# Kernel tuning notes

Hardware: AMD Instinct MI355X
Metric: run time of the kernel (lower is better)

The kernel has to match this reference:

```python
import jax, jax.numpy as jnp
from jax import lax
import numpy as np

D_MODEL = 512
H = 4
DK = 128
DV = 256
DFF = 2048
N_LAYERS = 12
N_LOC = 100  # 10x10 patches

CONV_SPECS = [(8, 3, 3), (16, 8, 3), (32, 16, 3), (32, 32, 3), (64, 32, 3),
              (64, 64, 3), (128, 64, 3), (128, 128, 3), (256, 128, 3), (512, 256, 2)]
RELU_AFTER = [False, True, False, True, True, True, True, True, True, False]


def setup_inputs() -> dict:
    key = jax.random.key(0)
    keys = iter(jax.random.split(key, 64))

    def nrm(shape, scale=0.02):
        return jax.random.normal(next(keys), shape, dtype=jnp.float32) * scale

    inp = {"x": jax.random.normal(next(keys), (1, 3, 200, 200), dtype=jnp.float32)}
    for i, (o, c, k) in enumerate(CONV_SPECS, 1):
        inp[f"cw{i}"] = nrm((o, c, k, k))
        inp[f"cb{i}"] = nrm((o,))
    inp["Wq"] = nrm((N_LAYERS, H, D_MODEL, DK))
    inp["Wk"] = nrm((N_LAYERS, H, D_MODEL, DK))
    inp["Wv"] = nrm((N_LAYERS, H, D_MODEL, DV))
    inp["Wo"] = nrm((N_LAYERS, H * DV, D_MODEL))
    inp["W1"] = nrm((N_LAYERS, D_MODEL, DFF))
    inp["b1"] = nrm((N_LAYERS, DFF))
    inp["W2"] = nrm((N_LAYERS, DFF, D_MODEL))
    inp["b2"] = nrm((N_LAYERS, D_MODEL))
    return inp


def _extract_patches(x):
    # x: [1,3,200,200] -> 100 patches of [3,20,20], index = i*10 + j
    # patch(i,j) = x[:, :, 20j:20(j+1), 20i:20(i+1)]  (i=cols outer, j=rows inner)
    x = x.reshape(3, 10, 20, 10, 20)            # [c, j_blk, row, i_blk, col]
    return jnp.transpose(x, (3, 1, 0, 2, 4)).reshape(N_LOC, 3, 20, 20)


def _local_embed(patches, cws, cbs):
    h = patches  # [100,3,20,20]
    for w, b, r in zip(cws, cbs, RELU_AFTER):
        h = lax.conv_general_dilated(h, w, (1, 1), 'VALID',
                                     dimension_numbers=('NCHW', 'OIHW', 'NCHW'))
        h = h + b[None, :, None, None]
        if r:
            h = jax.nn.relu(h)
    return h.reshape(N_LOC, D_MODEL)  # spatial reduced to 1x1


def _location_embeddings():
    # createLocationEmbedding(i, j) only uses i (the column-block coordinate).
    pos = jnp.repeat(jnp.arange(0, 200, 20, dtype=jnp.float32), 10)  # [100]
    k = jnp.arange(256, dtype=jnp.float32)
    inv = jnp.power(jnp.float32(10000.0), 2.0 * k / 256.0)
    ang = pos[:, None] / inv[None, :]  # [100,256]
    return jnp.concatenate([jnp.sin(ang), jnp.cos(ang)], axis=1)  # [100,512]


def _encoder_layer(h, Wq, Wk, Wv, Wo, W1, b1, W2, b2):
    # Multi-head attention; NOTE: scale uses K.size(0) = n_locations (faithful quirk).
    scale = 1.0 / jnp.sqrt(jnp.float32(N_LOC))
    q = jnp.einsum('nd,hdk->hnk', h, Wq)
    k = jnp.einsum('nd,hdk->hnk', h, Wk)
    v = jnp.einsum('nd,hdv->hnv', h, Wv)
    s = jnp.einsum('hnk,hmk->hnm', q, k) * scale
    a = jax.nn.softmax(s, axis=-1)
    o = jnp.einsum('hnm,hmv->hnv', a, v)
    o = jnp.transpose(o, (1, 0, 2)).reshape(N_LOC, H * DV)
    h = h + o @ Wo
    h = h + (jax.nn.relu(h @ W1 + b1) @ W2 + b2)
    return h


def reference(x, cw1, cb1, cw2, cb2, cw3, cb3, cw4, cb4, cw5, cb5,
              cw6, cb6, cw7, cb7, cw8, cb8, cw9, cb9, cw10, cb10,
              Wq, Wk, Wv, Wo, W1, b1, W2, b2):
    cws = [cw1, cw2, cw3, cw4, cw5, cw6, cw7, cw8, cw9, cw10]
    cbs = [cb1, cb2, cb3, cb4, cb5, cb6, cb7, cb8, cb9, cb10]
    patches = _extract_patches(x)
    h = _local_embed(patches, cws, cbs)
    h = h + _location_embeddings()
    for n in range(N_LAYERS):
        h = _encoder_layer(h, Wq[n], Wk[n], Wv[n], Wo[n], W1[n], b1[n], W2[n], b2[n])
    return h
```

## Files before the change

### kernel.cpp

```cpp
#include <hip/hip_runtime.h>
#include <math.h>

#define NLOC 100

typedef __attribute__((ext_vector_type(8))) _Float16 half8;
typedef __attribute__((ext_vector_type(4))) float f32x4;

#define XP_OFF    0
#define H_OFF     160000
#define QKV_OFF   211200
#define OCAT_OFF  416000
#define FFN_OFF   467200
#define ACTA_OFF  569600
#define ACTB_OFF  889664
#define CWH_OFF   1209728
#define CW1_OFF   1765504
#define WQKVT_OFF 1765824
#define WOT_OFF   8057280
#define W1T_OFF   11203008
#define W2T_OFF   17494464

struct WPack { const float* w[9]; };

__global__ __launch_bounds__(256) void stage_xp(const float* __restrict__ x, float* __restrict__ xp)
{
    int idx = blockIdx.x*256 + threadIdx.x;
    if (idx >= 160000) return;
    int c = idx & 3;
    int idx2 = idx >> 2;
    int p = idx2 / 400;
    int rr = idx2 - p*400;
    int y = rr / 20, xx = rr - y*20;
    int pi = p/10, pj = p - pi*10;
    float v = 0.f;
    if (c < 3) v = x[c*40000 + (pj*20 + y)*200 + pi*20 + xx];
    xp[idx] = v;
}

__global__ __launch_bounds__(256) void cw1repack(const float* __restrict__ w, float* __restrict__ w4)
{
    int idx = threadIdx.x;
    if (idx >= 288) return;
    int c = idx & 3;
    int r = idx >> 2;
    int oc = r / 9, kk = r - oc*9;
    int ky = kk/3, kx = kk - ky*3;
    float v = 0.f;
    if (c < 3) v = w[((oc*3 + c)*3 + ky)*3 + kx];
    w4[idx] = v;
}

__global__ __launch_bounds__(256) void cwrepack(WPack wp, unsigned short* __restrict__ dst)
{
    const int Cin[9]  = {8,16,32,32,64,64,128,128,256};
    const int shift[9]= {3,4,5,5,6,6,7,7,8};
    const int KS[9]   = {3,3,3,3,3,3,3,3,2};
    const int Kpad[9] = {96,160,288,288,576,576,1152,1152,1024};
    const int off[10] = {0,1536,6656,15872,34304,71168,144896,292352,587264,1111552};
    const int total = 1111552;
    for (int i = blockIdx.x*blockDim.x + threadIdx.x; i < total; i += gridDim.x*blockDim.x) {
        int l = 0;
        while (i >= off[l+1]) ++l;
        int rem = i - off[l];
        int kp = Kpad[l];
        int oc = rem / kp;
        int k  = rem - oc*kp;
        int ci = Cin[l];
        int ic = k & (ci - 1);
        int kk = k >> shift[l];
        int ks = KS[l], k2 = ks*ks;
        float v = 0.f;
        if (kk < k2) {
            int ky = kk / ks, kx = kk - ky*ks;
            v = wp.w[l][((oc*ci + ic)*ks + ky)*ks + kx];
        }
        _Float16 hv = (_Float16)v;
        dst[i] = __builtin_bit_cast(unsigned short, hv);
    }
}

__global__ __launch_bounds__(256) void conv1k(const float4* __restrict__ xp4,
    const float4* __restrict__ w4, const float* __restrict__ bias, unsigned short* __restrict__ out)
{
    int idx = blockIdx.x*256 + threadIdx.x;
    if (idx >= 259200) return;
    int oc = idx & 7;
    int r = idx >> 3;
    int p = r / 324;
    int s = r - p*324;
    int sy = s / 18, sx = s - sy*18;
    const float4* ip = xp4 + (size_t)(p*20 + sy)*20 + sx;
    float acc = 0.f;
    #pragma unroll
    for (int ky = 0; ky < 3; ++ky)
        #pragma unroll
        for (int kx = 0; kx < 3; ++kx) {
            float4 iv = ip[ky*20 + kx];
            float4 wv = w4[oc*9 + ky*3 + kx];
            acc += iv.x*wv.x + iv.y*wv.y + iv.z*wv.z;
        }
    acc += bias[oc];
    _Float16 hv = (_Float16)acc;
    out[idx] = __builtin_bit_cast(unsigned short, hv);
}

template<int CIN, int COUT, int KS, int HIN, int WIN, int HOUT, int WOUT, int KPAD, int RELU, int LAST>
__global__ __launch_bounds__(256) void convM(const unsigned short* __restrict__ in,
    const unsigned short* __restrict__ wth, const float* __restrict__ bias,
    unsigned short* __restrict__ out, float* __restrict__ hout)
{
    constexpr int HW = HOUT*WOUT;
    constexpr int M = 100*HW;
    constexpr int MT = (M + 15)/16;
    constexpr int NT = COUT/16;
    int wave = threadIdx.x >> 6, lane = threadIdx.x & 63;
    int t = blockIdx.x*4 + wave;
    if (t >= MT*NT) return;
    int mt = t % MT, nt = t / MT;
    int mrow = lane & 15, quad = lane >> 4;
    int mg = mt*16 + mrow; if (mg >= M) mg = M - 1;
    int p = mg / HW, s = mg - p*HW;
    int sy = s / WOUT, sx = s - sy*WOUT;
    const unsigned short* ap = in + ((size_t)((p*HIN + sy)*WIN + sx))*CIN;
    const unsigned short* bp = wth + ((size_t)(nt*16 + mrow))*KPAD + quad*8;
    f32x4 acc = {0.f, 0.f, 0.f, 0.f};
    #pragma unroll
    for (int k0 = 0; k0 < KPAD; k0 += 32) {
        int k = k0 + quad*8;
        int kk = k / CIN; if (kk > KS*KS - 1) kk = KS*KS - 1;
        int ky = kk / KS, kx = kk - ky*KS;
        uint4 av = *(const uint4*)(ap + (ky*WIN + kx)*CIN + (k & (CIN-1)));
        uint4 bv = *(const uint4*)(bp + k0);
        acc = __builtin_amdgcn_mfma_f32_16x16x32_f16(
            __builtin_bit_cast(half8, av), __builtin_bit_cast(half8, bv), acc, 0, 0, 0);
    }
    int n = nt*16 + mrow;
    float bv = bias[n];
    #pragma unroll
    for (int r = 0; r < 4; ++r) {
        int m = mt*16 + quad*4 + r;
        if (m < M) {
            float v = acc[r] + bv;
            if (RELU) v = fmaxf(v, 0.f);
            if (LAST) {
                int pi = m / 10;
                float pos = 20.f * (float)pi;
                int dd = n & 255;
                float inv = powf(10000.f, (float)dd * (1.f/128.f));
                float ang = pos / inv;
                v += (n < 256) ? sinf(ang) : cosf(ang);
                hout[(size_t)m*512 + n] = v;
            } else {
                _Float16 hv = (_Float16)v;
                out[(size_t)m*COUT + n] = __builtin_bit_cast(unsigned short, hv);
            }
        }
    }
}

__global__ __launch_bounds__(256) void wtrans(
    const float* __restrict__ src, unsigned short* __restrict__ dst,
    int K, int N, int matsPerLayer, int dstLayerStride, int dstBase)
{
    __shared__ float t[32][33];
    int mz = blockIdx.z;
    int layer = mz / matsPerLayer;
    int mi = mz - layer*matsPerLayer;
    const float* s = src + (size_t)mz * K * N;
    unsigned short* d = dst + (size_t)layer*dstLayerStride + dstBase + (size_t)mi * N * K;
    int n0 = blockIdx.x*32, k0 = blockIdx.y*32;
    int tx = threadIdx.x & 31, ty = threadIdx.x >> 5;
    #pragma unroll
    for (int i = 0; i < 32; i += 8) t[ty + i][tx] = s[(size_t)(k0 + ty + i)*N + n0 + tx];
    __syncthreads();
    #pragma unroll
    for (int i = 0; i < 32; i += 8) {
        _Float16 hv = (_Float16)t[tx][ty + i];
        d[(size_t)(n0 + ty + i)*K + k0 + tx] = __builtin_bit_cast(unsigned short, hv);
    }
}

template<int ABITS, int RELU, int ATOMIC, int STOREH>
__global__ __launch_bounds__(256) void gemm16(
    const void* __restrict__ Av, int lda,
    const unsigned short* __restrict__ Bt, int K,
    const float* __restrict__ bias,
    float* __restrict__ C, unsigned short* __restrict__ Ch, int ldc,
    int kchunk)
{
    int lane = threadIdx.x & 63;
    int wave = threadIdx.x >> 6;
    int mrow = lane & 15, quad = lane >> 4;
    int n0 = blockIdx.x*64 + wave*16;
    int m0 = blockIdx.y*16;
    int arow = m0 + mrow; if (arow > 99) arow = 99;
    int k0 = blockIdx.z * kchunk;
    const unsigned short* bp = Bt + (size_t)(n0 + mrow)*K + quad*8 + k0;
    f32x4 acc = {0.f, 0.f, 0.f, 0.f};
    if (ABITS == 16) {
        const unsigned short* ap = (const unsigned short*)Av + (size_t)arow*lda + quad*8 + k0;
        for (int k = 0; k < kchunk; k += 32) {
            uint4 au = *(const uint4*)(ap + k);
            uint4 bu = *(const uint4*)(bp + k);
            acc = __builtin_amdgcn_mfma_f32_16x16x32_f16(
                __builtin_bit_cast(half8, au), __builtin_bit_cast(half8, bu), acc, 0, 0, 0);
        }
    } else {
        const float* ap = (const float*)Av + (size_t)arow*lda + quad*8 + k0;
        for (int k = 0; k < kchunk; k += 32) {
            float4 f0 = *(const float4*)(ap + k);
            float4 f1 = *(const float4*)(ap + k + 4);
            half8 af;
            af[0] = (_Float16)f0.x; af[1] = (_Float16)f0.y;
            af[2] = (_Float16)f0.z; af[3] = (_Float16)f0.w;
            af[4] = (_Float16)f1.x; af[5] = (_Float16)f1.y;
            af[6] = (_Float16)f1.z; af[7] = (_Float16)f1.w;
            uint4 bu = *(const uint4*)(bp + k);
            acc = __builtin_amdgcn_mfma_f32_16x16x32_f16(
                af, __builtin_bit_cast(half8, bu), acc, 0, 0, 0);
        }
    }
    int n = n0 + mrow;
    float bv = (bias != nullptr && blockIdx.z == 0) ? bias[n] : 0.f;
    #pragma unroll
    for (int r = 0; r < 4; ++r) {
        int row = m0 + quad*4 + r;
        if (row < 100) {
            float v = acc[r] + bv;
            if (RELU) v = fmaxf(v, 0.f);
            if (ATOMIC) atomicAdd(&C[(size_t)row*ldc + n], v);
            else if (C != nullptr) C[(size_t)row*ldc + n] = v;
            if (STOREH) {
                _Float16 hv = (_Float16)v;
                Ch[(size_t)row*ldc + n] = __builtin_bit_cast(unsigned short, hv);
            }
        }
    }
}

__global__ __launch_bounds__(256) void attn_kernel(
    const float* __restrict__ qkv, unsigned short* __restrict__ ocat)
{
    __shared__ float qr[128];
    __shared__ float p[100];
    __shared__ float red[2];
    int bx = blockIdx.x;
    int hh = bx / 100, nn = bx - hh*100;
    int t = threadIdx.x;
    if (t < 128) qr[t] = qkv[(size_t)nn*2048 + hh*128 + t];
    __syncthreads();
    float sv = 0.f;
    if (t < 100) {
        const float4* kp = (const float4*)(qkv + (size_t)t*2048 + 512 + hh*128);
        const float4* q4 = (const float4*)qr;
        float s0=0.f, s1=0.f, s2=0.f, s3=0.f;
        #pragma unroll 8
        for (int j = 0; j < 32; ++j) {
            float4 a = q4[j], b = kp[j];
            s0 += a.x*b.x; s1 += a.y*b.y; s2 += a.z*b.z; s3 += a.w*b.w;
        }
        sv = (s0+s1+s2+s3) * 0.1f;
        p[t] = sv;
    }
    __syncthreads();
    if (t < 64) {
        float m = fmaxf(p[t], (t+64 < 100) ? p[t+64] : -1e30f);
        for (int o = 32; o > 0; o >>= 1) m = fmaxf(m, __shfl_down(m, o));
        if (t == 0) red[0] = m;
    }
    __syncthreads();
    float mx = red[0];
    if (t < 100) p[t] = expf(sv - mx);
    __syncthreads();
    if (t < 64) {
        float s = p[t] + ((t+64 < 100) ? p[t+64] : 0.f);
        for (int o = 32; o > 0; o >>= 1) s += __shfl_down(s, o);
        if (t == 0) red[1] = s;
    }
    __syncthreads();
    float inv = 1.0f / red[1];
    const float* vp = qkv + 1024 + hh*256 + t;
    float acc = 0.f;
    #pragma unroll 4
    for (int m = 0; m < 100; ++m) acc += p[m] * vp[(size_t)m*2048];
    _Float16 hv = (_Float16)(acc * inv);
    ocat[(size_t)nn*1024 + hh*256 + t] = __builtin_bit_cast(unsigned short, hv);
}

__global__ __launch_bounds__(256) void copyk(const float* __restrict__ s, float* __restrict__ d, int n)
{
    int i = blockIdx.x*256 + threadIdx.x;
    if (i < n) d[i] = s[i];
}

extern "C" void kernel_launch(void* const* d_in, const int* in_sizes, int n_in,
                              void* d_out, int out_size, void* d_ws, size_t ws_size,
                              hipStream_t stream)
{
    const float* x = (const float*)d_in[0];
    const float* cw1 = (const float*)d_in[1];
    const float* cb[10];
    WPack wpk;
    for (int i = 0; i < 10; ++i) cb[i] = (const float*)d_in[2 + 2*i];
    for (int i = 0; i < 9; ++i)  wpk.w[i] = (const float*)d_in[3 + 2*i];
    const float* Wq = (const float*)d_in[21];
    const float* Wk = (const float*)d_in[22];
    const float* Wv = (const float*)d_in[23];
    const float* Wo = (const float*)d_in[24];
    const float* W1 = (const float*)d_in[25];
    const float* b1 = (const float*)d_in[26];
    const float* W2 = (const float*)d_in[27];
    const float* b2 = (const float*)d_in[28];

    float* ws = (float*)d_ws;
    float* xp  = ws + XP_OFF;
    float* h   = ws + H_OFF;
    float* qkv = ws + QKV_OFF;
    unsigned short* ocat = (unsigned short*)(ws + OCAT_OFF);
    unsigned short* ffn  = (unsigned short*)(ws + FFN_OFF);
    unsigned short* aA   = (unsigned short*)(ws + ACTA_OFF);
    unsigned short* aB   = (unsigned short*)(ws + ACTB_OFF);
    unsigned short* cwh  = (unsigned short*)(ws + CWH_OFF);
    float* cw14 = ws + CW1_OFF;
    unsigned short* wqkvt = (unsigned short*)(ws + WQKVT_OFF);
    unsigned short* wot   = (unsigned short*)(ws + WOT_OFF);
    unsigned short* w1t   = (unsigned short*)(ws + W1T_OFF);
    unsigned short* w2t   = (unsigned short*)(ws + W2T_OFF);

    cw1repack<<<2, 256, 0, stream>>>(cw1, cw14);
    cwrepack<<<2172, 256, 0, stream>>>(wpk, cwh);
    wtrans<<<dim3(4, 16, 48),  256, 0, stream>>>(Wq, wqkvt, 512, 128,  4, 2048*512, 0);
    wtrans<<<dim3(4, 16, 48),  256, 0, stream>>>(Wk, wqkvt, 512, 128,  4, 2048*512, 512*512);
    wtrans<<<dim3(8, 16, 48),  256, 0, stream>>>(Wv, wqkvt, 512, 256,  4, 2048*512, 1024*512);
    wtrans<<<dim3(16, 32, 12), 256, 0, stream>>>(Wo, wot,  1024, 512,  1, 512*1024, 0);
    wtrans<<<dim3(64, 16, 12), 256, 0, stream>>>(W1, w1t,   512, 2048, 1, 2048*512, 0);
    wtrans<<<dim3(16, 64, 12), 256, 0, stream>>>(W2, w2t,  2048, 512,  1, 512*2048, 0);

    stage_xp<<<625, 256, 0, stream>>>(x, xp);
    conv1k<<<1013, 256, 0, stream>>>((const float4*)xp, (const float4*)cw14, cb[0], aA);
    convM<8,  16, 3,18,18,16,16,  96,1,0><<<400, 256, 0, stream>>>(aA, cwh + 0,      cb[1], aB, nullptr);
    convM<16, 32, 3,16,16,14,14, 160,0,0><<<613, 256, 0, stream>>>(aB, cwh + 1536,   cb[2], aA, nullptr);
    convM<32, 32, 3,14,14,12,12, 288,1,0><<<450, 256, 0, stream>>>(aA, cwh + 6656,   cb[3], aB, nullptr);
    convM<32, 64, 3,12,12,10,10, 288,1,0><<<625, 256, 0, stream>>>(aB, cwh + 15872,  cb[4], aA, nullptr);
    convM<64, 64, 3,10,10, 8, 8, 576,1,0><<<400, 256, 0, stream>>>(aA, cwh + 34304,  cb[5], aB, nullptr);
    convM<64,128, 3, 8, 8, 6, 6, 576,1,0><<<450, 256, 0, stream>>>(aB, cwh + 71168,  cb[6], aA, nullptr);
    convM<128,128,3, 6, 6, 4, 4,1152,1,0><<<200, 256, 0, stream>>>(aA, cwh + 144896, cb[7], aB, nullptr);
    convM<128,256,3, 4, 4, 2, 2,1152,1,0><<<100, 256, 0, stream>>>(aB, cwh + 292352, cb[8], aA, nullptr);
    convM<256,512,2, 2, 2, 1, 1,1024,0,1><<<56,  256, 0, stream>>>(aA, cwh + 587264, cb[9], nullptr, h);

    for (int n = 0; n < 12; ++n) {
        const unsigned short* Bq  = wqkvt + (size_t)n * 2048 * 512;
        const unsigned short* Bo  = wot   + (size_t)n * 512 * 1024;
        const unsigned short* Bf1 = w1t   + (size_t)n * 2048 * 512;
        const unsigned short* Bf2 = w2t   + (size_t)n * 512 * 2048;
        gemm16<32,0,0,0><<<dim3(32, 7, 1), 256, 0, stream>>>(h, 512, Bq, 512,
            nullptr, qkv, nullptr, 2048, 512);
        attn_kernel<<<400, 256, 0, stream>>>(qkv, ocat);
        gemm16<16,0,1,0><<<dim3(8, 7, 4), 256, 0, stream>>>(ocat, 1024, Bo, 1024,
            nullptr, h, nullptr, 512, 256);
        gemm16<32,1,0,1><<<dim3(32, 7, 1), 256, 0, stream>>>(h, 512, Bf1, 512,
            b1 + (size_t)n*2048, nullptr, ffn, 2048, 512);
        gemm16<16,0,1,0><<<dim3(8, 7, 8), 256, 0, stream>>>(ffn, 2048, Bf2, 2048,
            b2 + (size_t)n*512, h, nullptr, 512, 256);
    }
    copyk<<<200, 256, 0, stream>>>(h, (float*)d_out, NLOC*512);
}
```

Measured before the change: 880.8 us.

## Merge weight prep into one kernel, fuse attention with output projection

Replaces the conv weight repack and six transpose kernels with a single grid-stride prep kernel that transposes with vectorized stores. Folds patch staging into the first conv. Fuses attention with the Wo projection and residual add, using one 1024-thread block per query row. That block also writes an fp16 copy of h, so the FFN1 GEMM reads half-precision input. The aim is fewer launches and less intermediate traffic, but the fused Wo projection now runs as scalar FMAs over only 100 blocks instead of MFMA tiles.

Result: slower. 1.213 ms (+37.7%).

```diff
diff --git a/kernel.cpp b/kernel.cpp
--- a/kernel.cpp
+++ b/kernel.cpp
@@ -6,15 +6,13 @@
 typedef __attribute__((ext_vector_type(8))) _Float16 half8;
 typedef __attribute__((ext_vector_type(4))) float f32x4;
 
-#define XP_OFF    0
 #define H_OFF     160000
 #define QKV_OFF   211200
-#define OCAT_OFF  416000
+#define H16_OFF   416000
 #define FFN_OFF   467200
 #define ACTA_OFF  569600
 #define ACTB_OFF  889664
 #define CWH_OFF   1209728
-#define CW1_OFF   1765504
 #define WQKVT_OFF 1765824
 #define WOT_OFF   8057280
 #define W1T_OFF   11203008
@@ -22,66 +20,115 @@
 
 struct WPack { const float* w[9]; };
 
-__global__ __launch_bounds__(256) void stage_xp(const float* __restrict__ x, float* __restrict__ xp)
-{
-    int idx = blockIdx.x*256 + threadIdx.x;
-    if (idx >= 160000) return;
-    int c = idx & 3;
-    int idx2 = idx >> 2;
-    int p = idx2 / 400;
-    int rr = idx2 - p*400;
-    int y = rr / 20, xx = rr - y*20;
-    int pi = p/10, pj = p - pi*10;
-    float v = 0.f;
-    if (c < 3) v = x[c*40000 + (pj*20 + y)*200 + pi*20 + xx];
-    xp[idx] = v;
-}
-
-__global__ __launch_bounds__(256) void cw1repack(const float* __restrict__ w, float* __restrict__ w4)
-{
-    int idx = threadIdx.x;
-    if (idx >= 288) return;
-    int c = idx & 3;
-    int r = idx >> 2;
-    int oc = r / 9, kk = r - oc*9;
-    int ky = kk/3, kx = kk - ky*3;
-    float v = 0.f;
-    if (c < 3) v = w[((oc*3 + c)*3 + ky)*3 + kx];
-    w4[idx] = v;
-}
-
-__global__ __launch_bounds__(256) void cwrepack(WPack wp, unsigned short* __restrict__ dst)
-{
-    const int Cin[9]  = {8,16,32,32,64,64,128,128,256};
-    const int shift[9]= {3,4,5,5,6,6,7,7,8};
-    const int KS[9]   = {3,3,3,3,3,3,3,3,2};
-    const int Kpad[9] = {96,160,288,288,576,576,1152,1152,1024};
-    const int off[10] = {0,1536,6656,15872,34304,71168,144896,292352,587264,1111552};
-    const int total = 1111552;
-    for (int i = blockIdx.x*blockDim.x + threadIdx.x; i < total; i += gridDim.x*blockDim.x) {
-        int l = 0;
-        while (i >= off[l+1]) ++l;
-        int rem = i - off[l];
-        int kp = Kpad[l];
-        int oc = rem / kp;
-        int k  = rem - oc*kp;
-        int ci = Cin[l];
-        int ic = k & (ci - 1);
-        int kk = k >> shift[l];
-        int ks = KS[l], k2 = ks*ks;
+struct TJob {
+    const float* src; unsigned short* dst;
+    int K, N, mpl, lstride, base, tiles;
+};
+
+struct PrepParams {
+    WPack wpk;
+    const float* Wq; const float* Wk; const float* Wv; const float* Wo;
+    const float* W1; const float* W2;
+    float* ws;
+};
+
+__global__ __launch_bounds__(256) void prep_all(PrepParams PP)
+{
+    float* ws = PP.ws;
+    unsigned short* cwh   = (unsigned short*)(ws + CWH_OFF);
+    unsigned short* wqkvt = (unsigned short*)(ws + WQKVT_OFF);
+    unsigned short* wot   = (unsigned short*)(ws + WOT_OFF);
+    unsigned short* w1t   = (unsigned short*)(ws + W1T_OFF);
+    unsigned short* w2t   = (unsigned short*)(ws + W2T_OFF);
+
+    const int tid = threadIdx.x;
+    const int gthread = blockIdx.x*256 + tid;
+    const int nthreads = gridDim.x*256;
+    const int gwave = gthread >> 6;
+    const int nwaves = nthreads >> 6;
+    const int lane = tid & 63;
+
+    __shared__ TJob jobs[6];
+    if (tid == 0) {
+        jobs[0] = TJob{PP.Wq, wqkvt,  512,  128, 4, 2048*512, 0,        1536};
+        jobs[1] = TJob{PP.Wk, wqkvt,  512,  128, 4, 2048*512, 512*512,  1536};
+        jobs[2] = TJob{PP.Wv, wqkvt,  512,  256, 4, 2048*512, 1024*512, 3072};
+        jobs[3] = TJob{PP.Wo, wot,   1024,  512, 1, 512*1024, 0,        3072};
+        jobs[4] = TJob{PP.W1, w1t,    512, 2048, 1, 2048*512, 0,        6144};
+        jobs[5] = TJob{PP.W2, w2t,   2048,  512, 1, 512*2048, 0,        6144};
+    }
+    __syncthreads();
+
+    {
+        const int Cin[9]   = {8,16,32,32,64,64,128,128,256};
+        const int shiftv[9]= {3,4,5,5,6,6,7,7,8};
+        const int KSa[9]   = {3,3,3,3,3,3,3,3,2};
+        const int Kpad[9]  = {96,160,288,288,576,576,1152,1152,1024};
+        const int off[10]  = {0,1536,6656,15872,34304,71168,144896,292352,587264,1111552};
+        for (int i = gthread; i < 1111552; i += nthreads) {
+            int l = 0;
+            while (i >= off[l+1]) ++l;
+            int rem = i - off[l];
+            int kp = Kpad[l];
+            int oc = rem / kp;
+            int k  = rem - oc*kp;
+            int ci = Cin[l];
+            int ic = k & (ci - 1);
+            int kk = k >> shiftv[l];
+            int ks = KSa[l], k2 = ks*ks;
+            float v = 0.f;
+            if (kk < k2) {
+                int ky = kk / ks, kx = kk - ky*ks;
+                v = PP.wpk.w[l][((oc*ci + ic)*ks + ky)*ks + kx];
+            }
+            _Float16 hv = (_Float16)v;
+            cwh[i] = __builtin_bit_cast(unsigned short, hv);
+        }
+    }
+    for (int t = gwave; t < 21504; t += nwaves) {
+        int j = 0, rem = t;
+        while (rem >= jobs[j].tiles) { rem -= jobs[j].tiles; ++j; }
+        const int K = jobs[j].K, N = jobs[j].N;
+        const int nb = N >> 6, kb = K >> 5;
+        int mat = rem / (nb*kb);
+        int r2  = rem - mat*(nb*kb);
+        int n0  = (r2 % nb) << 6;
+        int k0  = (r2 / nb) << 5;
+        const float* s = jobs[j].src + (size_t)mat*K*N;
+        int layer = mat / jobs[j].mpl, mi = mat - layer*jobs[j].mpl;
+        unsigned short* d = jobs[j].dst + (size_t)layer*jobs[j].lstride + jobs[j].base + (size_t)mi*N*K;
+        int nn = n0 + lane;
+        #pragma unroll
+        for (int half = 0; half < 4; ++half) {
+            float v[8];
+            #pragma unroll
+            for (int kk = 0; kk < 8; ++kk) v[kk] = s[(size_t)(k0 + half*8 + kk)*N + nn];
+            unsigned int u[4];
+            #pragma unroll
+            for (int q = 0; q < 4; ++q) {
+                _Float16 a = (_Float16)v[2*q], b = (_Float16)v[2*q+1];
+                u[q] = (unsigned int)__builtin_bit_cast(unsigned short, a)
+                     | ((unsigned int)__builtin_bit_cast(unsigned short, b) << 16);
+            }
+            *(uint4*)(d + (size_t)nn*K + k0 + half*8) = make_uint4(u[0],u[1],u[2],u[3]);
+        }
+    }
+}
+
+__global__ __launch_bounds__(256) void conv1d(const float* __restrict__ x,
+    const float* __restrict__ cw1, const float* __restrict__ bias, unsigned short* __restrict__ out)
+{
+    __shared__ float w1s[288];
+    for (int i = threadIdx.x; i < 288; i += 256) {
+        int c = i & 3;
+        int r = i >> 2;
+        int oc = r / 9, kk = r - oc*9;
+        int ky = kk/3, kx = kk - ky*3;
         float v = 0.f;
-        if (kk < k2) {
-            int ky = kk / ks, kx = kk - ky*ks;
-            v = wp.w[l][((oc*ci + ic)*ks + ky)*ks + kx];
-        }
-        _Float16 hv = (_Float16)v;
-        dst[i] = __builtin_bit_cast(unsigned short, hv);
-    }
-}
-
-__global__ __launch_bounds__(256) void conv1k(const float4* __restrict__ xp4,
-    const float4* __restrict__ w4, const float* __restrict__ bias, unsigned short* __restrict__ out)
-{
+        if (c < 3) v = cw1[((oc*3 + c)*3 + ky)*3 + kx];
+        w1s[i] = v;
+    }
+    __syncthreads();
     int idx = blockIdx.x*256 + threadIdx.x;
     if (idx >= 259200) return;
     int oc = idx & 7;
@@ -89,16 +136,18 @@
     int p = r / 324;
     int s = r - p*324;
     int sy = s / 18, sx = s - sy*18;
-    const float4* ip = xp4 + (size_t)(p*20 + sy)*20 + sx;
+    int pi = p/10, pj = p - pi*10;
+    const float* xb = x + (size_t)(pj*20 + sy)*200 + pi*20 + sx;
     float acc = 0.f;
     #pragma unroll
-    for (int ky = 0; ky < 3; ++ky)
+    for (int c = 0; c < 3; ++c) {
+        const float* xc = xb + c*40000;
         #pragma unroll
-        for (int kx = 0; kx < 3; ++kx) {
-            float4 iv = ip[ky*20 + kx];
-            float4 wv = w4[oc*9 + ky*3 + kx];
-            acc += iv.x*wv.x + iv.y*wv.y + iv.z*wv.z;
-        }
+        for (int ky = 0; ky < 3; ++ky)
+            #pragma unroll
+            for (int kx = 0; kx < 3; ++kx)
+                acc += xc[ky*200 + kx] * w1s[(oc*9 + ky*3 + kx)*4 + c];
+    }
     acc += bias[oc];
     _Float16 hv = (_Float16)acc;
     out[idx] = __builtin_bit_cast(unsigned short, hv);
@@ -158,28 +207,6 @@
     }
 }
 
-__global__ __launch_bounds__(256) void wtrans(
-    const float* __restrict__ src, unsigned short* __restrict__ dst,
-    int K, int N, int matsPerLayer, int dstLayerStride, int dstBase)
-{
-    __shared__ float t[32][33];
-    int mz = blockIdx.z;
-    int layer = mz / matsPerLayer;
-    int mi = mz - layer*matsPerLayer;
-    const float* s = src + (size_t)mz * K * N;
-    unsigned short* d = dst + (size_t)layer*dstLayerStride + dstBase + (size_t)mi * N * K;
-    int n0 = blockIdx.x*32, k0 = blockIdx.y*32;
-    int tx = threadIdx.x & 31, ty = threadIdx.x >> 5;
-    #pragma unroll
-    for (int i = 0; i < 32; i += 8) t[ty + i][tx] = s[(size_t)(k0 + ty + i)*N + n0 + tx];
-    __syncthreads();
-    #pragma unroll
-    for (int i = 0; i < 32; i += 8) {
-        _Float16 hv = (_Float16)t[tx][ty + i];
-        d[(size_t)(n0 + ty + i)*K + k0 + tx] = __builtin_bit_cast(unsigned short, hv);
-    }
-}
-
 template<int ABITS, int RELU, int ATOMIC, int STOREH>
 __global__ __launch_bounds__(256) void gemm16(
     const void* __restrict__ Av, int lda,
@@ -238,21 +265,26 @@
     }
 }
 
-__global__ __launch_bounds__(256) void attn_kernel(
-    const float* __restrict__ qkv, unsigned short* __restrict__ ocat)
-{
-    __shared__ float qr[128];
-    __shared__ float p[100];
-    __shared__ float red[2];
-    int bx = blockIdx.x;
-    int hh = bx / 100, nn = bx - hh*100;
-    int t = threadIdx.x;
-    if (t < 128) qr[t] = qkv[(size_t)nn*2048 + hh*128 + t];
+__global__ __launch_bounds__(1024) void attn_fused(const float* __restrict__ qkv,
+    const unsigned short* __restrict__ Bo, float* __restrict__ h, unsigned short* __restrict__ h16)
+{
+    __shared__ float qs[512];
+    __shared__ float oc_s[1024];
+    __shared__ float pb[4][128];
+    __shared__ float rr[8];
+    const int nn = blockIdx.x;
+    const int tid = threadIdx.x;
+    const int hh = tid >> 8;
+    const int t  = tid & 255;
+    if (tid < 256) {
+        float2 qv = *(const float2*)(qkv + (size_t)nn*2048 + tid*2);
+        qs[tid*2] = qv.x; qs[tid*2 + 1] = qv.y;
+    }
     __syncthreads();
     float sv = 0.f;
     if (t < 100) {
+        const float4* q4 = (const float4*)(qs + hh*128);
         const float4* kp = (const float4*)(qkv + (size_t)t*2048 + 512 + hh*128);
-        const float4* q4 = (const float4*)qr;
         float s0=0.f, s1=0.f, s2=0.f, s3=0.f;
         #pragma unroll 8
         for (int j = 0; j < 32; ++j) {
@@ -260,31 +292,50 @@
             s0 += a.x*b.x; s1 += a.y*b.y; s2 += a.z*b.z; s3 += a.w*b.w;
         }
         sv = (s0+s1+s2+s3) * 0.1f;
-        p[t] = sv;
+        pb[hh][t] = sv;
     }
     __syncthreads();
     if (t < 64) {
-        float m = fmaxf(p[t], (t+64 < 100) ? p[t+64] : -1e30f);
+        float m = fmaxf(pb[hh][t], (t+64 < 100) ? pb[hh][t+64] : -1e30f);
         for (int o = 32; o > 0; o >>= 1) m = fmaxf(m, __shfl_down(m, o));
-        if (t == 0) red[0] = m;
-    }
-    __syncthreads();
-    float mx = red[0];
-    if (t < 100) p[t] = expf(sv - mx);
+        if (t == 0) rr[hh] = m;
+    }
+    __syncthreads();
+    float mx = rr[hh];
+    if (t < 100) pb[hh][t] = expf(sv - mx);
     __syncthreads();
     if (t < 64) {
-        float s = p[t] + ((t+64 < 100) ? p[t+64] : 0.f);
-        for (int o = 32; o > 0; o >>= 1) s += __shfl_down(s, o);
-        if (t == 0) red[1] = s;
-    }
-    __syncthreads();
-    float inv = 1.0f / red[1];
-    const float* vp = qkv + 1024 + hh*256 + t;
-    float acc = 0.f;
-    #pragma unroll 4
-    for (int m = 0; m < 100; ++m) acc += p[m] * vp[(size_t)m*2048];
-    _Float16 hv = (_Float16)(acc * inv);
-    ocat[(size_t)nn*1024 + hh*256 + t] = __builtin_bit_cast(unsigned short, hv);
+        float s2 = pb[hh][t] + ((t+64 < 100) ? pb[hh][t+64] : 0.f);
+        for (int o = 32; o > 0; o >>= 1) s2 += __shfl_down(s2, o);
+        if (t == 0) rr[4+hh] = s2;
+    }
+    __syncthreads();
+    float inv = 1.f / rr[4+hh];
+    {
+        const float* vp = qkv + 1024 + hh*256 + t;
+        float a0 = 0.f;
+        #pragma unroll 4
+        for (int m = 0; m < 100; ++m) a0 += pb[hh][m] * vp[(size_t)m*2048];
+        oc_s[hh*256 + t] = (float)(_Float16)(a0 * inv);
+    }
+    __syncthreads();
+    if (tid < 512) {
+        const unsigned short* wr = Bo + (size_t)tid*1024;
+        float acc = 0.f;
+        #pragma unroll 4
+        for (int k2 = 0; k2 < 1024; k2 += 8) {
+            uint4 wu = *(const uint4*)(wr + k2);
+            half8 wf = __builtin_bit_cast(half8, wu);
+            acc += oc_s[k2+0]*(float)wf[0] + oc_s[k2+1]*(float)wf[1]
+                 + oc_s[k2+2]*(float)wf[2] + oc_s[k2+3]*(float)wf[3]
+                 + oc_s[k2+4]*(float)wf[4] + oc_s[k2+5]*(float)wf[5]
+                 + oc_s[k2+6]*(float)wf[6] + oc_s[k2+7]*(float)wf[7];
+        }
+        float hv = h[(size_t)nn*512 + tid] + acc;
+        h[(size_t)nn*512 + tid] = hv;
+        _Float16 hf = (_Float16)hv;
+        h16[(size_t)nn*512 + tid] = __builtin_bit_cast(unsigned short, hf);
+    }
 }
 
 __global__ __launch_bounds__(256) void copyk(const float* __restrict__ s, float* __restrict__ d, int n)
@@ -313,31 +364,25 @@
     const float* b2 = (const float*)d_in[28];
 
     float* ws = (float*)d_ws;
-    float* xp  = ws + XP_OFF;
     float* h   = ws + H_OFF;
     float* qkv = ws + QKV_OFF;
-    unsigned short* ocat = (unsigned short*)(ws + OCAT_OFF);
+    unsigned short* h16  = (unsigned short*)(ws + H16_OFF);
     unsigned short* ffn  = (unsigned short*)(ws + FFN_OFF);
     unsigned short* aA   = (unsigned short*)(ws + ACTA_OFF);
     unsigned short* aB   = (unsigned short*)(ws + ACTB_OFF);
     unsigned short* cwh  = (unsigned short*)(ws + CWH_OFF);
-    float* cw14 = ws + CW1_OFF;
     unsigned short* wqkvt = (unsigned short*)(ws + WQKVT_OFF);
     unsigned short* wot   = (unsigned short*)(ws + WOT_OFF);
     unsigned short* w1t   = (unsigned short*)(ws + W1T_OFF);
     unsigned short* w2t   = (unsigned short*)(ws + W2T_OFF);
 
-    cw1repack<<<2, 256, 0, stream>>>(cw1, cw14);
-    cwrepack<<<2172, 256, 0, stream>>>(wpk, cwh);
-    wtrans<<<dim3(4, 16, 48),  256, 0, stream>>>(Wq, wqkvt, 512, 128,  4, 2048*512, 0);
-    wtrans<<<dim3(4, 16, 48),  256, 0, stream>>>(Wk, wqkvt, 512, 128,  4, 2048*512, 512*512);
-    wtrans<<<dim3(8, 16, 48),  256, 0, stream>>>(Wv, wqkvt, 512, 256,  4, 2048*512, 1024*512);
-    wtrans<<<dim3(16, 32, 12), 256, 0, stream>>>(Wo, wot,  1024, 512,  1, 512*1024, 0);
-    wtrans<<<dim3(64, 16, 12), 256, 0, stream>>>(W1, w1t,   512, 2048, 1, 2048*512, 0);
-    wtrans<<<dim3(16, 64, 12), 256, 0, stream>>>(W2, w2t,  2048, 512,  1, 512*2048, 0);
-
-    stage_xp<<<625, 256, 0, stream>>>(x, xp);
-    conv1k<<<1013, 256, 0, stream>>>((const float4*)xp, (const float4*)cw14, cb[0], aA);
+    PrepParams PP;
+    PP.wpk = wpk;
+    PP.Wq = Wq; PP.Wk = Wk; PP.Wv = Wv; PP.Wo = Wo; PP.W1 = W1; PP.W2 = W2;
+    PP.ws = ws;
+    prep_all<<<2048, 256, 0, stream>>>(PP);
+
+    conv1d<<<1013, 256, 0, stream>>>(x, cw1, cb[0], aA);
     convM<8,  16, 3,18,18,16,16,  96,1,0><<<400, 256, 0, stream>>>(aA, cwh + 0,      cb[1], aB, nullptr);
     convM<16, 32, 3,16,16,14,14, 160,0,0><<<613, 256, 0, stream>>>(aB, cwh + 1536,   cb[2], aA, nullptr);
     convM<32, 32, 3,14,14,12,12, 288,1,0><<<450, 256, 0, stream>>>(aA, cwh + 6656,   cb[3], aB, nullptr);
@@ -355,10 +400,8 @@
         const unsigned short* Bf2 = w2t   + (size_t)n * 512 * 2048;
         gemm16<32,0,0,0><<<dim3(32, 7, 1), 256, 0, stream>>>(h, 512, Bq, 512,
             nullptr, qkv, nullptr, 2048, 512);
-        attn_kernel<<<400, 256, 0, stream>>>(qkv, ocat);
-        gemm16<16,0,1,0><<<dim3(8, 7, 4), 256, 0, stream>>>(ocat, 1024, Bo, 1024,
-            nullptr, h, nullptr, 512, 256);
-        gemm16<32,1,0,1><<<dim3(32, 7, 1), 256, 0, stream>>>(h, 512, Bf1, 512,
+        attn_fused<<<100, 1024, 0, stream>>>(qkv, Bo, h, h16);
+        gemm16<16,1,0,1><<<dim3(32, 7, 1), 256, 0, stream>>>(h16, 512, Bf1, 512,
             b1 + (size_t)n*2048, nullptr, ffn, 2048, 512);
         gemm16<16,0,1,0><<<dim3(8, 7, 8), 256, 0, stream>>>(ffn, 2048, Bf2, 2048,
             b2 + (size_t)n*512, h, nullptr, 512, 256);
```
